# Kernel optimization log

Hardware: AMD Instinct MI355X
Metric: run time of the kernel (lower is better)

## Reference

```python
import jax, jax.numpy as jnp
import numpy as np

IN_SHAPE_DOWN = (8, 16, 8)   # prod = 1024
OUT_SHAPE_DOWN = (4, 4, 4)   # prod = 64
TT_RANK = 8


def tt_to_dense(cores, in_shape, out_shape):
    """Contract TT-matrix cores [r_{k-1}, i_k, j_k, r_k] into a dense (prod_in, prod_out) matrix."""
    res = cores[0]  # [1, i1, j1, r1]
    for c in cores[1:]:
        res = jnp.einsum('...a,aijb->...ijb', res, c)
    res = res[0, ..., 0]  # (i1, j1, i2, j2, ..., id, jd)
    d = len(in_shape)
    perm = [2 * k for k in range(d)] + [2 * k + 1 for k in range(d)]
    return res.transpose(perm).reshape(int(np.prod(in_shape)), int(np.prod(out_shape)))


def setup_inputs() -> dict:
    key = jax.random.key(0)
    ks = jax.random.split(key, 8)
    r = TT_RANK
    # down cores: in factors (8,16,8) -> out factors (4,4,4)
    d1 = 0.1 * jax.random.normal(ks[0], (1, 8, 4, r), dtype=jnp.float32)
    d2 = 0.1 * jax.random.normal(ks[1], (r, 16, 4, r), dtype=jnp.float32)
    d3 = 0.1 * jax.random.normal(ks[2], (r, 8, 4, 1), dtype=jnp.float32)
    # up cores: shape = [reversed(out_down), reversed(in_down)] = [(4,4,4),(8,16,8)]
    u1 = 0.1 * jax.random.normal(ks[3], (1, 4, 8, r), dtype=jnp.float32)
    u2 = 0.1 * jax.random.normal(ks[4], (r, 4, 16, r), dtype=jnp.float32)
    u3 = 0.1 * jax.random.normal(ks[5], (r, 4, 8, 1), dtype=jnp.float32)
    x = jax.random.normal(ks[6], (4, 4096, 1024), dtype=jnp.float32)
    bias_down = 0.001 * jnp.ones((64,), dtype=jnp.float32)
    bias_up = 0.001 * jnp.ones((1024,), dtype=jnp.float32)
    return {"x": x, "d1": d1, "d2": d2, "d3": d3,
            "u1": u1, "u2": u2, "u3": u3,
            "bias_down": bias_down, "bias_up": bias_up}


def reference(x, d1, d2, d3, u1, u2, u3, bias_down, bias_up):
    # Down-project TT matrix: 1024 -> 64
    Wd = tt_to_dense([d1, d2, d3], IN_SHAPE_DOWN, OUT_SHAPE_DOWN)
    # Up-project TT matrix: 64 -> 1024 (reversed factor shapes)
    Wu = tt_to_dense([u1, u2, u3], tuple(reversed(OUT_SHAPE_DOWN)), tuple(reversed(IN_SHAPE_DOWN)))
    z = jnp.einsum('bsd,dk->bsk', x, Wd) + bias_down
    z = jax.nn.relu(z)
    y = jnp.einsum('bsk,kd->bsd', z, Wu) + bias_up
    return y
```

## Files before the change

### kernel.cpp

```cpp
#include <hip/hip_runtime.h>

typedef float f32x2 __attribute__((ext_vector_type(2)));
typedef float f32x4 __attribute__((ext_vector_type(4)));
typedef short short8 __attribute__((ext_vector_type(8)));

static __device__ __forceinline__ unsigned short f2bf(float f) {
    __bf16 h = (__bf16)f;
    return __builtin_bit_cast(unsigned short, h);
}

static __device__ __forceinline__ void gload_lds16(const void* g, void* l) {
    __builtin_amdgcn_global_load_lds(
        (const __attribute__((address_space(1))) void*)g,
        (__attribute__((address_space(3))) void*)l, 16, 0, 0);
}

__global__ __launch_bounds__(256) void tt_build_w_kernel(
    const float* __restrict__ d1, const float* __restrict__ d2, const float* __restrict__ d3,
    const float* __restrict__ u1, const float* __restrict__ u2, const float* __restrict__ u3,
    unsigned short* __restrict__ WdT_sw, unsigned short* __restrict__ WuT_sw)
{
    int t = blockIdx.x * 256 + threadIdx.x;
    if (t < 65536) {
        int j = t >> 10, i = t & 1023;
        int i1 = i >> 7, i2 = (i >> 3) & 15, i3 = i & 7;
        int j1 = j >> 4, j2 = (j >> 2) & 3, j3 = j & 3;
        float t3[8];
#pragma unroll
        for (int b = 0; b < 8; ++b) t3[b] = d3[(b * 8 + i3) * 4 + j3];
        float wsum = 0.f;
#pragma unroll
        for (int a = 0; a < 8; ++a) {
            float va = d1[(i1 * 4 + j1) * 8 + a];
            const float* p2 = d2 + ((a * 16 + i2) * 4 + j2) * 8;
            float wa = 0.f;
#pragma unroll
            for (int b = 0; b < 8; ++b) wa = fmaf(p2[b], t3[b], wa);
            wsum = fmaf(va, wa, wsum);
        }
        int q_ = i >> 8, ck = (i >> 6) & 3, ks2 = (i >> 5) & 1;
        int kg_ = (i >> 3) & 3, m = i & 7;
        int off = (q_ * 4 + ck) * 4096 + ((ks2 * 4 + kg_) * 64 + j) * 8 + m;
        WdT_sw[off] = f2bf(wsum);
    } else {
        int t2 = t - 65536;
        int d = t2 >> 6, k = t2 & 63;
        int k1 = k >> 4, k2 = (k >> 2) & 3, k3 = k & 3;
        int o1 = d >> 7, o2 = (d >> 3) & 15, o3 = d & 7;
        float t3[8];
#pragma unroll
        for (int b = 0; b < 8; ++b) t3[b] = u3[(b * 4 + k3) * 8 + o3];
        float wsum = 0.f;
#pragma unroll
        for (int a = 0; a < 8; ++a) {
            float va = u1[(k1 * 8 + o1) * 8 + a];
            const float* p2 = u2 + ((a * 4 + k2) * 16 + o2) * 8;
            float wa = 0.f;
#pragma unroll
            for (int b = 0; b < 8; ++b) wa = fmaf(p2[b], t3[b], wa);
            wsum = fmaf(va, wa, wsum);
        }
        int dl = d & 511, hf = d >> 9;
        int off = hf * 32768 + (dl * 8 + ((k >> 3) ^ (dl & 7))) * 8 + (k & 7);
        WuT_sw[off] = f2bf(wsum);
    }
}

__global__ __launch_bounds__(256) void tt_gemm1_kernel(
    const float* __restrict__ x, const unsigned short* __restrict__ WdT_sw,
    const float* __restrict__ bd, unsigned short* __restrict__ zbuf)
{
    __shared__ float red[4][4][1024];
    const int t = threadIdx.x;
    const int lane = t & 63;
    const int h = t >> 6;
    const int l15 = lane & 15;
    const int kg = lane >> 4;
    const int tile0 = blockIdx.x * 4;

    const int colz = (t >> 6) * 16 + (t & 15);
    const int rowz = ((t & 63) >> 4) * 4;
    const float bdv = bd[colz];

    const float* xp0 = x + ((size_t)(tile0 + 0) * 16 + l15) * 1024 + h * 256 + kg * 8;
    const float* xp1 = xp0 + 16 * 1024;
    const float* xp2 = xp0 + 32 * 1024;
    const float* xp3 = xp0 + 48 * 1024;
    const unsigned short* wqb = WdT_sw + h * 16384 + kg * 512 + l15 * 8;
    const unsigned short* wq0 = wqb;
    const unsigned short* wq1 = wqb + 2048;
    const unsigned short* wq2 = wqb + 4096;
    const unsigned short* wq3 = wqb + 6144;
    const unsigned short* wq4 = wqb + 8192;
    const unsigned short* wq5 = wqb + 10240;
    const unsigned short* wq6 = wqb + 12288;
    const unsigned short* wq7 = wqb + 14336;

    f32x4 xA[8], xB[8];
    short8 wA[4], wB[4];
    f32x4 acc[4][4];
#pragma unroll
    for (int t4 = 0; t4 < 4; ++t4)
#pragma unroll
        for (int ct = 0; ct < 4; ++ct) acc[t4][ct] = {0.f, 0.f, 0.f, 0.f};

#define ISSUE(D, W, WQ, O0, O1)                                                                   \
    asm volatile("global_load_dwordx4 %0, %1, off offset:" #O0 : "=v"(D[0]) : "v"(xp0) : "memory"); \
    asm volatile("global_load_dwordx4 %0, %1, off offset:" #O1 : "=v"(D[1]) : "v"(xp0) : "memory"); \
    asm volatile("global_load_dwordx4 %0, %1, off offset:" #O0 : "=v"(D[2]) : "v"(xp1) : "memory"); \
    asm volatile("global_load_dwordx4 %0, %1, off offset:" #O1 : "=v"(D[3]) : "v"(xp1) : "memory"); \
    asm volatile("global_load_dwordx4 %0, %1, off offset:" #O0 : "=v"(D[4]) : "v"(xp2) : "memory"); \
    asm volatile("global_load_dwordx4 %0, %1, off offset:" #O1 : "=v"(D[5]) : "v"(xp2) : "memory"); \
    asm volatile("global_load_dwordx4 %0, %1, off offset:" #O0 : "=v"(D[6]) : "v"(xp3) : "memory"); \
    asm volatile("global_load_dwordx4 %0, %1, off offset:" #O1 : "=v"(D[7]) : "v"(xp3) : "memory"); \
    asm volatile("global_load_dwordx4 %0, %1, off offset:0"   : "=v"(W[0]) : "v"(WQ) : "memory");   \
    asm volatile("global_load_dwordx4 %0, %1, off offset:256" : "=v"(W[1]) : "v"(WQ) : "memory");   \
    asm volatile("global_load_dwordx4 %0, %1, off offset:512" : "=v"(W[2]) : "v"(WQ) : "memory");   \
    asm volatile("global_load_dwordx4 %0, %1, off offset:768" : "=v"(W[3]) : "v"(WQ) : "memory");

#define CPT(D, W, WN) do {                                                                   \
    asm volatile("s_waitcnt vmcnt(" #WN ")" ::: "memory");                                   \
    __builtin_amdgcn_sched_barrier(0);                                                       \
    _Pragma("unroll")                                                                        \
    for (int t4 = 0; t4 < 4; ++t4) {                                                         \
        union { short8 v; unsigned short e[8]; } a;                                          \
        _Pragma("unroll")                                                                    \
        for (int e = 0; e < 4; ++e) {                                                        \
            a.e[e]     = f2bf(D[2 * t4][e]);                                                 \
            a.e[e + 4] = f2bf(D[2 * t4 + 1][e]);                                             \
        }                                                                                    \
        _Pragma("unroll")                                                                    \
        for (int ct = 0; ct < 4; ++ct)                                                       \
            acc[t4][ct] = __builtin_amdgcn_mfma_f32_16x16x32_bf16(a.v, W[ct], acc[t4][ct],   \
                                                                  0, 0, 0);                  \
    }                                                                                        \
    __builtin_amdgcn_sched_barrier(0);                                                       \
} while (0)

    ISSUE(xA, wA, wq0, 0, 16)
    ISSUE(xB, wB, wq1, 128, 144)
    CPT(xA, wA, 12); ISSUE(xA, wA, wq2, 256, 272)
    CPT(xB, wB, 12); ISSUE(xB, wB, wq3, 384, 400)
    CPT(xA, wA, 12); ISSUE(xA, wA, wq4, 512, 528)
    CPT(xB, wB, 12); ISSUE(xB, wB, wq5, 640, 656)
    CPT(xA, wA, 12); ISSUE(xA, wA, wq6, 768, 784)
    CPT(xB, wB, 12); ISSUE(xB, wB, wq7, 896, 912)
    CPT(xA, wA, 12);
    CPT(xB, wB, 0);
#undef ISSUE
#undef CPT

#pragma unroll
    for (int t4 = 0; t4 < 4; ++t4)
#pragma unroll
        for (int ct = 0; ct < 4; ++ct)
            *reinterpret_cast<f32x4*>(&red[t4][h][ct * 256 + lane * 4]) = acc[t4][ct];
    __syncthreads();
#pragma unroll
    for (int t4 = 0; t4 < 4; ++t4) {
        f32x4 v0 = *reinterpret_cast<const f32x4*>(&red[t4][0][t * 4]);
        f32x4 v1 = *reinterpret_cast<const f32x4*>(&red[t4][1][t * 4]);
        f32x4 v2 = *reinterpret_cast<const f32x4*>(&red[t4][2][t * 4]);
        f32x4 v3 = *reinterpret_cast<const f32x4*>(&red[t4][3][t * 4]);
        const int tile = tile0 + t4;
#pragma unroll
        for (int r = 0; r < 4; ++r) {
            float zz = v0[r] + v1[r] + v2[r] + v3[r] + bdv;
            zz = zz > 0.f ? zz : 0.f;
            zbuf[tile * 1024 + (rowz + r) * 64 + colz] = f2bf(zz);
        }
    }
}

__global__ __launch_bounds__(256) void tt_gemm2_kernel(
    const unsigned short* __restrict__ zbuf, const unsigned short* __restrict__ WuT_sw,
    const float* __restrict__ bu, float* __restrict__ y)
{
    __shared__ unsigned short wlds2[32768];
    const int t = threadIdx.x;
    const int lane = t & 63;
    const int w = t >> 6;
    const int l15 = lane & 15;
    const int kg = lane >> 4;
    const int ch = blockIdx.x & 1;
    const int rg = blockIdx.x >> 1;

    const unsigned short* src = WuT_sw + ch * 32768 + w * 8192 + lane * 8;
#pragma unroll
    for (int i = 0; i < 16; ++i)
        gload_lds16(src + i * 512, &wlds2[w * 8192 + i * 512]);

    f32x4 bv[8];
#pragma unroll
    for (int i = 0; i < 8; ++i)
        bv[i] = *reinterpret_cast<const f32x4*>(bu + ch * 512 + w * 128 + i * 16 + kg * 4);
    __syncthreads();

#pragma unroll
    for (int tt = 0; tt < 8; ++tt) {
        const int tile = rg * 8 + tt;
        short8 az0 = *reinterpret_cast<const short8*>(zbuf + tile * 1024 + l15 * 64 + kg * 8);
        short8 az1 = *reinterpret_cast<const short8*>(zbuf + tile * 1024 + l15 * 64 + 32 + kg * 8);
        const size_t yb = (size_t)(tile * 16 + l15) * 1024 + ch * 512 + w * 128;
#pragma unroll
        for (int i = 0; i < 8; ++i) {
            const int row = w * 128 + i * 16 + l15;
            const int s = row & 7;
            short8 b0 = *reinterpret_cast<const short8*>(&wlds2[(row * 8 + (kg ^ s)) * 8]);
            short8 b1 = *reinterpret_cast<const short8*>(&wlds2[(row * 8 + ((kg + 4) ^ s)) * 8]);
            f32x4 c = {0.f, 0.f, 0.f, 0.f};
            c = __builtin_amdgcn_mfma_f32_16x16x32_bf16(b0, az0, c, 0, 0, 0);
            c = __builtin_amdgcn_mfma_f32_16x16x32_bf16(b1, az1, c, 0, 0, 0);
            f32x4 o;
#pragma unroll
            for (int r = 0; r < 4; ++r) o[r] = c[r] + bv[i][r];
            *reinterpret_cast<f32x4*>(y + yb + i * 16 + kg * 4) = o;
        }
    }
}

extern "C" void kernel_launch(void* const* d_in, const int* in_sizes, int n_in,
                              void* d_out, int out_size, void* d_ws, size_t ws_size,
                              hipStream_t stream) {
    const float* x  = (const float*)d_in[0];
    const float* d1 = (const float*)d_in[1];
    const float* d2 = (const float*)d_in[2];
    const float* d3 = (const float*)d_in[3];
    const float* u1 = (const float*)d_in[4];
    const float* u2 = (const float*)d_in[5];
    const float* u3 = (const float*)d_in[6];
    const float* bd = (const float*)d_in[7];
    const float* bu = (const float*)d_in[8];
    float* y = (float*)d_out;
    unsigned short* WdT_sw = (unsigned short*)d_ws;
    unsigned short* WuT_sw = WdT_sw + 65536;
    unsigned short* zbuf   = WuT_sw + 65536;

    hipLaunchKernelGGL(tt_build_w_kernel, dim3(512), dim3(256), 0, stream,
                       d1, d2, d3, u1, u2, u3, WdT_sw, WuT_sw);
    hipLaunchKernelGGL(tt_gemm1_kernel, dim3(256), dim3(256), 0, stream,
                       x, WdT_sw, bd, zbuf);
    hipLaunchKernelGGL(tt_gemm2_kernel, dim3(256), dim3(256), 0, stream,
                       zbuf, WuT_sw, bu, y);
}
```

Measured before the change: 35.76 us.

## Fuse down-projection and up-projection GEMMs into one kernel via LDS

Merges the two GEMM kernels so each block keeps its ReLU'd bf16 activation tile in shared memory (padded stride 80) instead of writing it to a global buffer and reloading it. The up-projection weights are loaded into the reused reduction buffer in two halves per block, and the block then writes the full output rows. This removes one kernel launch and the global round trip of the intermediate. In exchange, each block now loads the whole up-weight matrix, adds extra barriers, and does more serial work per block.

```diff
diff --git a/kernel.cpp b/kernel.cpp
--- a/kernel.cpp
+++ b/kernel.cpp
@@ -66,11 +66,13 @@
     }
 }
 
-__global__ __launch_bounds__(256) void tt_gemm1_kernel(
+__global__ __launch_bounds__(256) void tt_fused_kernel(
     const float* __restrict__ x, const unsigned short* __restrict__ WdT_sw,
-    const float* __restrict__ bd, unsigned short* __restrict__ zbuf)
+    const unsigned short* __restrict__ WuT_sw, const float* __restrict__ bd,
+    const float* __restrict__ bu, float* __restrict__ y)
 {
     __shared__ float red[4][4][1024];
+    __shared__ unsigned short zlds[4][16 * 80];
     const int t = threadIdx.x;
     const int lane = t & 63;
     const int h = t >> 6;
@@ -162,60 +164,51 @@
         f32x4 v1 = *reinterpret_cast<const f32x4*>(&red[t4][1][t * 4]);
         f32x4 v2 = *reinterpret_cast<const f32x4*>(&red[t4][2][t * 4]);
         f32x4 v3 = *reinterpret_cast<const f32x4*>(&red[t4][3][t * 4]);
-        const int tile = tile0 + t4;
 #pragma unroll
         for (int r = 0; r < 4; ++r) {
             float zz = v0[r] + v1[r] + v2[r] + v3[r] + bdv;
             zz = zz > 0.f ? zz : 0.f;
-            zbuf[tile * 1024 + (rowz + r) * 64 + colz] = f2bf(zz);
+            zlds[t4][(rowz + r) * 80 + colz] = f2bf(zz);
         }
     }
-}
-
-__global__ __launch_bounds__(256) void tt_gemm2_kernel(
-    const unsigned short* __restrict__ zbuf, const unsigned short* __restrict__ WuT_sw,
-    const float* __restrict__ bu, float* __restrict__ y)
-{
-    __shared__ unsigned short wlds2[32768];
-    const int t = threadIdx.x;
-    const int lane = t & 63;
-    const int w = t >> 6;
-    const int l15 = lane & 15;
-    const int kg = lane >> 4;
-    const int ch = blockIdx.x & 1;
-    const int rg = blockIdx.x >> 1;
-
-    const unsigned short* src = WuT_sw + ch * 32768 + w * 8192 + lane * 8;
-#pragma unroll
-    for (int i = 0; i < 16; ++i)
-        gload_lds16(src + i * 512, &wlds2[w * 8192 + i * 512]);
-
-    f32x4 bv[8];
-#pragma unroll
-    for (int i = 0; i < 8; ++i)
-        bv[i] = *reinterpret_cast<const f32x4*>(bu + ch * 512 + w * 128 + i * 16 + kg * 4);
     __syncthreads();
 
-#pragma unroll
-    for (int tt = 0; tt < 8; ++tt) {
-        const int tile = rg * 8 + tt;
-        short8 az0 = *reinterpret_cast<const short8*>(zbuf + tile * 1024 + l15 * 64 + kg * 8);
-        short8 az1 = *reinterpret_cast<const short8*>(zbuf + tile * 1024 + l15 * 64 + 32 + kg * 8);
-        const size_t yb = (size_t)(tile * 16 + l15) * 1024 + ch * 512 + w * 128;
-#pragma unroll
-        for (int i = 0; i < 8; ++i) {
-            const int row = w * 128 + i * 16 + l15;
-            const int s = row & 7;
-            short8 b0 = *reinterpret_cast<const short8*>(&wlds2[(row * 8 + (kg ^ s)) * 8]);
-            short8 b1 = *reinterpret_cast<const short8*>(&wlds2[(row * 8 + ((kg + 4) ^ s)) * 8]);
-            f32x4 c = {0.f, 0.f, 0.f, 0.f};
-            c = __builtin_amdgcn_mfma_f32_16x16x32_bf16(b0, az0, c, 0, 0, 0);
-            c = __builtin_amdgcn_mfma_f32_16x16x32_bf16(b1, az1, c, 0, 0, 0);
-            f32x4 o;
-#pragma unroll
-            for (int r = 0; r < 4; ++r) o[r] = c[r] + bv[i][r];
-            *reinterpret_cast<f32x4*>(y + yb + i * 16 + kg * 4) = o;
-        }
+    unsigned short* wlds = reinterpret_cast<unsigned short*>(&red[0][0][0]);
+    const int w = h;
+#pragma unroll
+    for (int ch = 0; ch < 2; ++ch) {
+        const unsigned short* src = WuT_sw + ch * 32768 + w * 8192 + lane * 8;
+#pragma unroll
+        for (int i = 0; i < 16; ++i)
+            gload_lds16(src + i * 512, wlds + w * 8192 + i * 512);
+        f32x4 bv[8];
+#pragma unroll
+        for (int i = 0; i < 8; ++i)
+            bv[i] = *reinterpret_cast<const f32x4*>(bu + ch * 512 + w * 128 + i * 16 + kg * 4);
+        __syncthreads();
+
+#pragma unroll
+        for (int tt = 0; tt < 4; ++tt) {
+            const int tile = tile0 + tt;
+            short8 az0 = *reinterpret_cast<const short8*>(&zlds[tt][l15 * 80 + kg * 8]);
+            short8 az1 = *reinterpret_cast<const short8*>(&zlds[tt][l15 * 80 + 32 + kg * 8]);
+            const size_t yb = (size_t)(tile * 16 + l15) * 1024 + ch * 512 + w * 128;
+#pragma unroll
+            for (int i = 0; i < 8; ++i) {
+                const int row = w * 128 + i * 16 + l15;
+                const int s = row & 7;
+                short8 b0 = *reinterpret_cast<const short8*>(&wlds[(row * 8 + (kg ^ s)) * 8]);
+                short8 b1 = *reinterpret_cast<const short8*>(&wlds[(row * 8 + ((kg + 4) ^ s)) * 8]);
+                f32x4 c = {0.f, 0.f, 0.f, 0.f};
+                c = __builtin_amdgcn_mfma_f32_16x16x32_bf16(b0, az0, c, 0, 0, 0);
+                c = __builtin_amdgcn_mfma_f32_16x16x32_bf16(b1, az1, c, 0, 0, 0);
+                f32x4 o;
+#pragma unroll
+                for (int r = 0; r < 4; ++r) o[r] = c[r] + bv[i][r];
+                *reinterpret_cast<f32x4*>(y + yb + i * 16 + kg * 4) = o;
+            }
+        }
+        __syncthreads();
     }
 }
 
@@ -234,12 +227,9 @@
     float* y = (float*)d_out;
     unsigned short* WdT_sw = (unsigned short*)d_ws;
     unsigned short* WuT_sw = WdT_sw + 65536;
-    unsigned short* zbuf   = WuT_sw + 65536;
 
     hipLaunchKernelGGL(tt_build_w_kernel, dim3(512), dim3(256), 0, stream,
                        d1, d2, d3, u1, u2, u3, WdT_sw, WuT_sw);
-    hipLaunchKernelGGL(tt_gemm1_kernel, dim3(256), dim3(256), 0, stream,
-                       x, WdT_sw, bd, zbuf);
-    hipLaunchKernelGGL(tt_gemm2_kernel, dim3(256), dim3(256), 0, stream,
-                       zbuf, WuT_sw, bu, y);
-}
+    hipLaunchKernelGGL(tt_fused_kernel, dim3(256), dim3(256), 0, stream,
+                       x, WdT_sw, WuT_sw, bd, bu, y);
+}
```

New measurement: 33.66 us. -5.9%, faster.
